# Kernel tuning notes

Measured on AMD Instinct MI355X. Metric: run time of the kernel, lower is better.

## Reference

```python
import jax, jax.numpy as jnp
import numpy as np

# ---- module config (from init_kwargs) ----
KERNEL_SIZE = 3
DIM = 3
HALF = KERNEL_SIZE // 2          # kernel offsets span [-HALF, HALF]
COORD_RANGE = 256                # voxel grid extent per spatial axis
NUM_BATCH = 4
N_VOXELS = 100_000
FEAT_DIM = 32
STRIDE = COORD_RANGE + 2 * HALF  # encoding stride so shifted coords fit


def _kernel_offsets():
    # All offsets of a KERNEL_SIZE^DIM kernel, centered (MinkowskiEngine-style).
    r = np.arange(-HALF, HALF + 1)
    grids = np.meshgrid(*([r] * DIM), indexing='ij')
    return jnp.asarray(np.stack([g.ravel() for g in grids], axis=1), dtype=jnp.int32)  # [K, DIM]


def setup_inputs() -> dict:
    key = jax.random.key(0)
    k1, k2, k3 = jax.random.split(key, 3)
    batch = jax.random.randint(k1, (1, N_VOXELS), 0, NUM_BATCH, dtype=jnp.int32)
    coords = jax.random.randint(k2, (3, N_VOXELS), 0, COORD_RANGE, dtype=jnp.int32)
    sparse_indices = jnp.concatenate([batch, coords], axis=0)  # [4, N]
    features = jax.random.normal(k3, (N_VOXELS, FEAT_DIM), dtype=jnp.float32)
    return {"sparse_indices": sparse_indices, "features": features}


def _kernel_map_and_out_key(sparse_indices):
    offsets = _kernel_offsets()                 # [K, 3]
    K = offsets.shape[0]
    b = sparse_indices[0].astype(jnp.int32)     # [N]
    coords = sparse_indices[1:].T.astype(jnp.int32)  # [N, 3]
    N = coords.shape[0]
    NK = N * K

    # neighbor coords per (voxel, offset); shift by HALF so values are >= 0
    nbr = coords[:, None, :] + offsets[None, :, :] + HALF     # [N, K, 3]
    S = STRIDE
    # unique integer hash of (batch, x, y, z); fits in int32 for these ranges
    enc = ((b[:, None] * S + nbr[..., 0]) * S + nbr[..., 1]) * S + nbr[..., 2]
    enc = enc.reshape(-1)                                     # [NK]

    # unique keys (sorted) + inverse map; pad to static size NK
    uniq, inv = jnp.unique(enc, return_inverse=True, size=NK, fill_value=-1)

    # reorder unique keys into first-seen order to match the dict-based reference
    first = jnp.full((NK,), NK, dtype=jnp.int32).at[inv].min(
        jnp.arange(NK, dtype=jnp.int32))
    order = jnp.argsort(first)                                # padding sorts last
    new_id = jnp.zeros((NK,), dtype=jnp.int32).at[order].set(
        jnp.arange(NK, dtype=jnp.int32))
    out_idx = new_id[inv]                                     # [NK] output index per entry

    # decode unique (first-seen ordered) keys back to spatial coords
    uo = uniq[order]
    valid = uo >= 0
    z = uo % S
    y = (uo // S) % S
    x = (uo // (S * S)) % S
    out_key = jnp.stack([x, y, z], axis=1) - HALF             # undo shift
    out_key = jnp.where(valid[:, None], out_key, -1)          # [NK, 3], padded rows = -1

    input_idx = jnp.repeat(jnp.arange(N, dtype=jnp.int32), K) # [NK]
    rel_pos = jnp.tile(jnp.arange(K, dtype=jnp.int32), N)     # [NK]
    kernel_map = jnp.stack([input_idx, out_idx, rel_pos], axis=1)  # [NK, 3]
    return kernel_map, out_key


def reference(sparse_indices, features):
    kernel_map, out_key = _kernel_map_and_out_key(sparse_indices)
    NK = kernel_map.shape[0]
    # canonical downstream use of the kernel map: gather inputs, scatter-sum to outputs
    out_feats = jax.ops.segment_sum(features[kernel_map[:, 0]],
                                    kernel_map[:, 1], num_segments=NK)
    return kernel_map, out_key, out_feats
```

## Files before the change

### kernel.cpp

```cpp
#include <hip/hip_runtime.h>
#include <stdint.h>

typedef unsigned long long u64;
typedef unsigned u32;
typedef float __attribute__((ext_vector_type(4))) f4raw;

#define K 27
#define S 258
#define ENCMAX (4 * S * S * S)

__device__ __forceinline__ void gbar(int* cnt, int nblk) {
    __syncthreads();
    if (threadIdx.x == 0) {
        __threadfence();
        __hip_atomic_fetch_add(cnt, 1, __ATOMIC_RELEASE, __HIP_MEMORY_SCOPE_AGENT);
        while (__hip_atomic_load(cnt, __ATOMIC_RELAXED, __HIP_MEMORY_SCOPE_AGENT) < nblk)
            __builtin_amdgcn_s_sleep(2);
        (void)__hip_atomic_load(cnt, __ATOMIC_ACQUIRE, __HIP_MEMORY_SCOPE_AGENT);
        __threadfence();
    }
    __syncthreads();
}

__global__ void k_mark(const int* __restrict__ si, int N,
                       u64* __restrict__ bits, u64* __restrict__ dupb) {
    int idx = blockIdx.x * blockDim.x + threadIdx.x;
    if (idx >= N * 9) return;
    int n = idx / 9, run = idx - n * 9;
    int ox = run / 3, oy = run - ox * 3;
    int b = si[n], x = si[N + n], y = si[2 * N + n], z = si[3 * N + n];
    unsigned enc0 = (unsigned)(((b * S + x + ox) * S + (y + oy)) * S + z);
    unsigned w = enc0 >> 6; int bit = enc0 & 63;
    u64 m1 = 7ull << bit;
    u64 old = atomicOr(&bits[w], m1);
    u64 d1 = old & m1;
    if (d1) atomicOr(&dupb[w], d1);
    if (bit > 61) {
        u64 m2 = 7ull >> (64 - bit);
        u64 old2 = atomicOr(&bits[w + 1], m2);
        u64 d2 = old2 & m2;
        if (d2) atomicOr(&dupb[w + 1], d2);
    }
}

__global__ void __launch_bounds__(256, 2)
k_s13(const u64* __restrict__ bits, const u64* __restrict__ dupb,
      int* __restrict__ tsums, u64* __restrict__ gt, int* __restrict__ barcnt) {
    __shared__ int s[256];
    int tid = threadIdx.x;
    int b = blockIdx.x;
    size_t wb = (size_t)b * 4096 + (size_t)tid * 16;
    u64 bb[16]; int pc[16]; int tsum = 0;
#pragma unroll
    for (int j = 0; j < 16; j++) { bb[j] = bits[wb + j]; pc[j] = __popcll(bb[j]); tsum += pc[j]; }
    s[tid] = tsum; __syncthreads();
    for (int off = 128; off > 0; off >>= 1) {
        if (tid < off) s[tid] += s[tid + off];
        __syncthreads();
    }
    if (tid == 0) tsums[b] = s[0];
    gbar(barcnt, gridDim.x);
    int pre = 0;
    for (int j = tid; j < b; j += 256) pre += tsums[j];
    s[tid] = pre; __syncthreads();
    for (int off = 128; off > 0; off >>= 1) {
        if (tid < off) s[tid] += s[tid + off];
        __syncthreads();
    }
    int tbase = s[0]; __syncthreads();
    s[tid] = tsum; __syncthreads();
    for (int off = 1; off < 256; off <<= 1) {
        int t = (tid >= off) ? s[tid - off] : 0;
        __syncthreads();
        s[tid] += t;
        __syncthreads();
    }
    int run = tbase + s[tid] - tsum;
#pragma unroll
    for (int j = 0; j < 16; j++) {
        u32 dup = (dupb[wb + j] != 0ull) ? 0x80000000u : 0u;
        gt[2 * (wb + j)]     = bb[j];
        gt[2 * (wb + j) + 1] = (u64)((u32)run | dup);
        run += pc[j];
    }
}

__global__ void k_kid(const int* __restrict__ si, int N,
                      const u64* __restrict__ gt,
                      int* __restrict__ kid, int* __restrict__ minE) {
    int idx = blockIdx.x * blockDim.x + threadIdx.x;
    if (idx >= N * 9) return;
    int n = idx / 9, run = idx - n * 9;
    int ox = run / 3, oy = run - ox * 3;
    int b = si[n], x = si[N + n], y = si[2 * N + n], z = si[3 * N + n];
    unsigned enc0 = (unsigned)(((b * S + x + ox) * S + (y + oy)) * S + z);
    unsigned w = enc0 >> 6; int bit = enc0 & 63;
    ulonglong2 r0 = *(const ulonglong2*)(gt + 2 * (size_t)w);
    u64 bb0 = r0.x; u32 q0 = (u32)r0.y;
    u64 bb1 = 0; u32 q1 = 0;
    if (bit > 61) {
        ulonglong2 r1 = *(const ulonglong2*)(gt + 2 * (size_t)(w + 1));
        bb1 = r1.x; q1 = (u32)r1.y;
    }
    int e0 = n * K + run * 3;
#pragma unroll
    for (int oz = 0; oz < 3; ++oz) {
        unsigned enc = enc0 + oz;
        int bit2 = enc & 63;
        bool hi = (enc >> 6) != w;
        u64 bbw = hi ? bb1 : bb0;
        u32 q   = hi ? q1 : q0;
        int kd = (int)(q & 0x7FFFFFFFu) + __popcll(bbw & ((1ull << bit2) - 1));
        int multi = (int)(q >> 31);
        kid[e0 + oz] = multi ? (int)((u32)kd | 0x80000000u) : kd;
        if (multi) atomicMin(&minE[kd], e0 + oz);
    }
}

__global__ void k_flagsum(const int* __restrict__ kid, const int* __restrict__ minE,
                          int NK, int* __restrict__ bsums) {
    __shared__ int s[256];
    int tid = threadIdx.x;
    int base = blockIdx.x * 4096 + tid * 16;
    int kv[16];
    *(int4*)(kv + 0)  = *(const int4*)(kid + base + 0);
    *(int4*)(kv + 4)  = *(const int4*)(kid + base + 4);
    *(int4*)(kv + 8)  = *(const int4*)(kid + base + 8);
    *(int4*)(kv + 12) = *(const int4*)(kid + base + 12);
    int sum = 0;
#pragma unroll
    for (int j = 0; j < 16; j++) {
        int e = base + j;
        if (e < NK) {
            int v = kv[j];
            sum += (v >= 0) ? 1 : (minE[v & 0x7FFFFFFF] == e ? 1 : 0);
        }
    }
    s[tid] = sum; __syncthreads();
    for (int off = 128; off > 0; off >>= 1) {
        if (tid < off) s[tid] += s[tid + off];
        __syncthreads();
    }
    if (tid == 0) bsums[blockIdx.x] = s[0];
}

__global__ void k_scanC(int* __restrict__ kid, const int* __restrict__ minE,
                        const int* __restrict__ bsums, const int* __restrict__ si,
                        int N, int NK, int NB,
                        float* __restrict__ out_key, int* __restrict__ rank_key,
                        float4* __restrict__ outF4) {
    __shared__ int s[256];
    __shared__ u64 s2[256];
    int tid = threadIdx.x;
    u64 acc = 0;
    for (int j = tid; j < NB; j += 256) {
        u64 b = (u64)(u32)bsums[j];
        acc += b << 32;
        if (j < (int)blockIdx.x) acc += b;
    }
    s2[tid] = acc; __syncthreads();
    for (int off = 128; off > 0; off >>= 1) {
        if (tid < off) s2[tid] += s2[tid + off];
        __syncthreads();
    }
    int blockoff = (int)(u32)(s2[0] & 0xFFFFFFFFull);
    int U = (int)(s2[0] >> 32);

    int base = blockIdx.x * 4096 + tid * 16;
    int kv[16];
    *(int4*)(kv + 0)  = *(const int4*)(kid + base + 0);
    *(int4*)(kv + 4)  = *(const int4*)(kid + base + 4);
    *(int4*)(kv + 8)  = *(const int4*)(kid + base + 8);
    *(int4*)(kv + 12) = *(const int4*)(kid + base + 12);
    int fbits = 0;
#pragma unroll
    for (int j = 0; j < 16; j++) {
        int e = base + j;
        int f = 0;
        if (e < NK) {
            int v = kv[j];
            f = (v >= 0) ? 1 : (minE[v & 0x7FFFFFFF] == e ? 1 : 0);
        }
        fbits |= f << j;
    }
    int tsum = __popc(fbits);
    s[tid] = tsum; __syncthreads();
    for (int off = 1; off < 256; off <<= 1) {
        int t = (tid >= off) ? s[tid - off] : 0;
        __syncthreads();
        s[tid] += t;
        __syncthreads();
    }
    int offset = blockoff + s[tid] - tsum;
    float4 zf = {0.f, 0.f, 0.f, 0.f};
    int run = 0;
#pragma unroll
    for (int j = 0; j < 16; j++) {
        int e = base + j;
        if ((fbits >> j) & 1) {
            int rank = offset + run;
            int n = e / K; int m = e - n * K;
            int x = si[N + n], y = si[2 * N + n], z = si[3 * N + n];
            int ox = m / 9; int rm = m - ox * 9; int oy = rm / 3; int oz = rm - oy * 3;
            out_key[(size_t)rank * 3 + 0] = (float)(x + ox - 1);
            out_key[(size_t)rank * 3 + 1] = (float)(y + oy - 1);
            out_key[(size_t)rank * 3 + 2] = (float)(z + oz - 1);
            int v = kv[j];
            if (v < 0) {
                int kd = v & 0x7FFFFFFF;
                rank_key[kd] = rank;
                kid[e] = rank | 0x40000000;
                float4* q = outF4 + (size_t)rank * 8;
#pragma unroll
                for (int q8 = 0; q8 < 8; q8++) q[q8] = zf;
            } else {
                kid[e] = rank;
            }
            run++;
        }
    }
    int rows = NK - U;
    int gs = gridDim.x * blockDim.x;
    for (int i = blockIdx.x * blockDim.x + tid; i < rows; i += gs) {
        int row = U + i;
        float4* q = outF4 + (size_t)row * 8;
#pragma unroll
        for (int q8 = 0; q8 < 8; q8++) q[q8] = zf;
        out_key[(size_t)row * 3 + 0] = -1.0f;
        out_key[(size_t)row * 3 + 1] = -1.0f;
        out_key[(size_t)row * 3 + 2] = -1.0f;
    }
}

__global__ void k_final(const int* __restrict__ ent, const int* __restrict__ rank_key,
                        const float4* __restrict__ feat4,
                        float* __restrict__ km, float* __restrict__ outF, int NK) {
    int total = NK * 8;
    int gs = gridDim.x * blockDim.x;
    for (int idx = blockIdx.x * blockDim.x + threadIdx.x; idx < total; idx += gs) {
        int e = idx >> 3, g = idx & 7;
        int v = ent[e];
        int n = e / K, m = e - n * K;
        float4 val = feat4[(size_t)n * 8 + g];
        int uid, atom;
        if (v < 0)                { uid = rank_key[v & 0x7FFFFFFF]; atom = 1; }
        else if (v & 0x40000000)  { uid = v & 0x3FFFFFFF;           atom = 1; }
        else                      { uid = v;                        atom = 0; }
        float* dst = outF + (size_t)uid * 32 + g * 4;
        if (atom) {
            atomicAdd(dst + 0, val.x);
            atomicAdd(dst + 1, val.y);
            atomicAdd(dst + 2, val.z);
            atomicAdd(dst + 3, val.w);
        } else {
            f4raw vr = {val.x, val.y, val.z, val.w};
            __builtin_nontemporal_store(vr, (f4raw*)dst);
        }
        if (g < 3)
            km[(size_t)e * 3 + g] = (g == 0) ? (float)n
                                   : ((g == 1) ? (float)uid : (float)m);
    }
}

extern "C" void kernel_launch(void* const* d_in, const int* in_sizes, int n_in,
                              void* d_out, int out_size, void* d_ws, size_t ws_size,
                              hipStream_t stream) {
    const int* si = (const int*)d_in[0];
    const float4* feat4 = (const float4*)d_in[1];
    int N = in_sizes[0] / 4;
    int NK = N * K;
    int NKp = (NK + 4095) & ~4095;
    int NB = NKp / 4096;

    int NW = (ENCMAX + 63) / 64;
    int NT = (NW + 4095) / 4096;
    int NWp = NT * 4096;

    float* km = (float*)d_out;
    float* out_key = km + (size_t)NK * 3;
    float* outF = km + (size_t)NK * 6;

    char* w = (char*)d_ws;
    char* p_bar   = w; w += 64;
    char* p_bits  = w; w += ((size_t)NWp * 8 + 15) & ~(size_t)15;
    char* p_dupb  = w; w += ((size_t)NWp * 8 + 15) & ~(size_t)15;
    size_t zbytes = (size_t)(w - (char*)d_ws);
    char* p_gt    = w; w += ((size_t)NWp * 16 + 15) & ~(size_t)15;
    char* p_tsums = w; w += ((size_t)(NT + 1) * 4 + 15) & ~(size_t)15;
    char* p_minE  = w; w += ((size_t)NK * 4 + 15) & ~(size_t)15;
    char* p_kid   = w; w += ((size_t)NKp * 4 + 15) & ~(size_t)15;
    char* p_rank  = w; w += ((size_t)NK * 4 + 15) & ~(size_t)15;
    char* p_bsums = w; w += ((size_t)(NB + 1) * 4 + 15) & ~(size_t)15;

    int* barcnt   = (int*)p_bar;
    u64* bits     = (u64*)p_bits;
    u64* dupb     = (u64*)p_dupb;
    u64* gt       = (u64*)p_gt;
    int* tsums    = (int*)p_tsums;
    int* minE     = (int*)p_minE;
    int* kid      = (int*)p_kid;
    int* rank_key = (int*)p_rank;
    int* bsums    = (int*)p_bsums;

    (void)hipMemsetAsync(d_ws, 0, zbytes, stream);
    (void)hipMemsetAsync(minE, 0x7F, (size_t)NK * 4, stream);

    int nb9 = (N * 9 + 255) / 256;
    k_mark<<<nb9, 256, 0, stream>>>(si, N, bits, dupb);
    k_s13<<<NT, 256, 0, stream>>>(bits, dupb, tsums, gt, barcnt);
    k_kid<<<nb9, 256, 0, stream>>>(si, N, gt, kid, minE);
    k_flagsum<<<NB, 256, 0, stream>>>(kid, minE, NK, bsums);
    k_scanC<<<NB, 256, 0, stream>>>(kid, minE, bsums, si, N, NK, NB,
                                    out_key, rank_key, (float4*)outF);
    k_final<<<2048, 256, 0, stream>>>(kid, rank_key, feat4, km, outF, NK);
}
```

Measured before the change: 636.1 us.

## Replace interleaved bitmap table with compact prefix array and fuse minE init

The scan kernel no longer copies the 64-bit occupancy words into a 16-byte-per-word table. It writes only a 4-byte per-word prefix with a duplicate flag, and the lookup kernel reads bits, prefix and (conditionally) dupb separately. The per-bit duplicate test now uses the dupb bit for the exact position instead of a per-word flag, which marks fewer entries as multi and avoids unneeded atomics. The minE initialization memset is folded into the scan kernel. This cuts a large write of about 4x the bitmap size, at the cost of more scattered separate loads in k_kid.

After: 601.4 us. -5.5%, faster.

```diff
diff --git a/kernel.cpp b/kernel.cpp
--- a/kernel.cpp
+++ b/kernel.cpp
@@ -45,14 +45,19 @@
 
 __global__ void __launch_bounds__(256, 2)
 k_s13(const u64* __restrict__ bits, const u64* __restrict__ dupb,
-      int* __restrict__ tsums, u64* __restrict__ gt, int* __restrict__ barcnt) {
+      int* __restrict__ tsums, u32* __restrict__ wprefix,
+      int* __restrict__ minE, int NK, int* __restrict__ barcnt) {
     __shared__ int s[256];
+    __shared__ int tb;
     int tid = threadIdx.x;
     int b = blockIdx.x;
+    int gs = gridDim.x * 256;
+    for (int i = b * 256 + tid; i < NK; i += gs) minE[i] = 0x7F7F7F7F;
+
     size_t wb = (size_t)b * 4096 + (size_t)tid * 16;
-    u64 bb[16]; int pc[16]; int tsum = 0;
-#pragma unroll
-    for (int j = 0; j < 16; j++) { bb[j] = bits[wb + j]; pc[j] = __popcll(bb[j]); tsum += pc[j]; }
+    int pc[16]; int tsum = 0;
+#pragma unroll
+    for (int j = 0; j < 16; j++) { pc[j] = __popcll(bits[wb + j]); tsum += pc[j]; }
     s[tid] = tsum; __syncthreads();
     for (int off = 128; off > 0; off >>= 1) {
         if (tid < off) s[tid] += s[tid + off];
@@ -67,7 +72,9 @@
         if (tid < off) s[tid] += s[tid + off];
         __syncthreads();
     }
-    int tbase = s[0]; __syncthreads();
+    if (tid == 0) tb = s[0];
+    __syncthreads();
+    int tbase = tb;
     s[tid] = tsum; __syncthreads();
     for (int off = 1; off < 256; off <<= 1) {
         int t = (tid >= off) ? s[tid - off] : 0;
@@ -79,14 +86,14 @@
 #pragma unroll
     for (int j = 0; j < 16; j++) {
         u32 dup = (dupb[wb + j] != 0ull) ? 0x80000000u : 0u;
-        gt[2 * (wb + j)]     = bb[j];
-        gt[2 * (wb + j) + 1] = (u64)((u32)run | dup);
+        wprefix[wb + j] = (u32)run | dup;
         run += pc[j];
     }
 }
 
 __global__ void k_kid(const int* __restrict__ si, int N,
-                      const u64* __restrict__ gt,
+                      const u64* __restrict__ bits, const u64* __restrict__ dupb,
+                      const u32* __restrict__ wprefix,
                       int* __restrict__ kid, int* __restrict__ minE) {
     int idx = blockIdx.x * blockDim.x + threadIdx.x;
     if (idx >= N * 9) return;
@@ -95,12 +102,12 @@
     int b = si[n], x = si[N + n], y = si[2 * N + n], z = si[3 * N + n];
     unsigned enc0 = (unsigned)(((b * S + x + ox) * S + (y + oy)) * S + z);
     unsigned w = enc0 >> 6; int bit = enc0 & 63;
-    ulonglong2 r0 = *(const ulonglong2*)(gt + 2 * (size_t)w);
-    u64 bb0 = r0.x; u32 q0 = (u32)r0.y;
-    u64 bb1 = 0; u32 q1 = 0;
+    u64 bw0 = bits[w]; u32 q0 = wprefix[w];
+    u64 db0 = (q0 & 0x80000000u) ? dupb[w] : 0ull;
+    u64 bw1 = 0, db1 = 0; u32 q1 = 0;
     if (bit > 61) {
-        ulonglong2 r1 = *(const ulonglong2*)(gt + 2 * (size_t)(w + 1));
-        bb1 = r1.x; q1 = (u32)r1.y;
+        bw1 = bits[w + 1]; q1 = wprefix[w + 1];
+        db1 = (q1 & 0x80000000u) ? dupb[w + 1] : 0ull;
     }
     int e0 = n * K + run * 3;
 #pragma unroll
@@ -108,10 +115,11 @@
         unsigned enc = enc0 + oz;
         int bit2 = enc & 63;
         bool hi = (enc >> 6) != w;
-        u64 bbw = hi ? bb1 : bb0;
+        u64 bwx = hi ? bw1 : bw0;
+        u64 dbx = hi ? db1 : db0;
         u32 q   = hi ? q1 : q0;
-        int kd = (int)(q & 0x7FFFFFFFu) + __popcll(bbw & ((1ull << bit2) - 1));
-        int multi = (int)(q >> 31);
+        int kd = (int)(q & 0x7FFFFFFFu) + __popcll(bwx & ((1ull << bit2) - 1));
+        int multi = (int)((dbx >> bit2) & 1);
         kid[e0 + oz] = multi ? (int)((u32)kd | 0x80000000u) : kd;
         if (multi) atomicMin(&minE[kd], e0 + oz);
     }
@@ -285,8 +293,8 @@
     char* p_bits  = w; w += ((size_t)NWp * 8 + 15) & ~(size_t)15;
     char* p_dupb  = w; w += ((size_t)NWp * 8 + 15) & ~(size_t)15;
     size_t zbytes = (size_t)(w - (char*)d_ws);
-    char* p_gt    = w; w += ((size_t)NWp * 16 + 15) & ~(size_t)15;
     char* p_tsums = w; w += ((size_t)(NT + 1) * 4 + 15) & ~(size_t)15;
+    char* p_wpref = w; w += ((size_t)NWp * 4 + 15) & ~(size_t)15;
     char* p_minE  = w; w += ((size_t)NK * 4 + 15) & ~(size_t)15;
     char* p_kid   = w; w += ((size_t)NKp * 4 + 15) & ~(size_t)15;
     char* p_rank  = w; w += ((size_t)NK * 4 + 15) & ~(size_t)15;
@@ -295,20 +303,19 @@
     int* barcnt   = (int*)p_bar;
     u64* bits     = (u64*)p_bits;
     u64* dupb     = (u64*)p_dupb;
-    u64* gt       = (u64*)p_gt;
     int* tsums    = (int*)p_tsums;
+    u32* wprefix  = (u32*)p_wpref;
     int* minE     = (int*)p_minE;
     int* kid      = (int*)p_kid;
     int* rank_key = (int*)p_rank;
     int* bsums    = (int*)p_bsums;
 
     (void)hipMemsetAsync(d_ws, 0, zbytes, stream);
-    (void)hipMemsetAsync(minE, 0x7F, (size_t)NK * 4, stream);
 
     int nb9 = (N * 9 + 255) / 256;
     k_mark<<<nb9, 256, 0, stream>>>(si, N, bits, dupb);
-    k_s13<<<NT, 256, 0, stream>>>(bits, dupb, tsums, gt, barcnt);
-    k_kid<<<nb9, 256, 0, stream>>>(si, N, gt, kid, minE);
+    k_s13<<<NT, 256, 0, stream>>>(bits, dupb, tsums, wprefix, minE, NK, barcnt);
+    k_kid<<<nb9, 256, 0, stream>>>(si, N, bits, dupb, wprefix, kid, minE);
     k_flagsum<<<NB, 256, 0, stream>>>(kid, minE, NK, bsums);
     k_scanC<<<NB, 256, 0, stream>>>(kid, minE, bsums, si, N, NK, NB,
                                     out_key, rank_key, (float4*)outF);
```
